# Optimization experiments

Measured on AMD Instinct MI355X. Metric: run time of the kernel, lower is better.

The kernel has to match this reference:

```python
import jax, jax.numpy as jnp
import numpy as np

K_FACTOR = 8
TOP_N = 4
NUM_LAYER = 2


def setup_inputs() -> dict:
    key = jax.random.key(0)
    ks = jax.random.split(key, 5)
    num_ent, num_rel, n_edges = 50000, 500, 500000
    emb_dim = 128
    emb_s = emb_dim // K_FACTOR  # 16
    ent_embeddings = jax.random.normal(ks[0], (num_ent, emb_dim), jnp.float32)
    rel_embeddings = jax.random.normal(ks[1], (num_rel, TOP_N * emb_s), jnp.float32)
    rel_att = jax.random.normal(ks[2], (num_rel, K_FACTOR), jnp.float32)
    edge_index = jax.random.randint(ks[3], (2, n_edges), 0, num_ent)
    edge_type = jax.random.randint(ks[4], (n_edges,), 0, num_rel)
    return dict(ent_embeddings=ent_embeddings, rel_embeddings=rel_embeddings,
                rel_att=rel_att, edge_index=edge_index, edge_type=edge_type,
                num_ent=num_ent, num_rel=num_rel)


def _segment_mean(src, idx, n):
    s = jax.ops.segment_sum(src, idx, num_segments=n)
    c = jax.ops.segment_sum(jnp.ones((src.shape[0],), src.dtype), idx, num_segments=n)
    return jnp.where(c[:, None] > 0, s / jnp.maximum(c, 1.0)[:, None], 0.0)


def _conv(x, r, r_att, ei, et, num_ent, num_rel):
    emb_dim = x.shape[1]
    s = emb_dim // K_FACTOR
    # add self-loop edges with relation id num_rel (zero embedding / zero att)
    loop = jnp.arange(num_ent, dtype=ei.dtype)
    ei = jnp.concatenate([ei, jnp.stack([loop, loop])], axis=1)
    et = jnp.concatenate([et, jnp.full((num_ent,), num_rel, et.dtype)])
    r_pad = jnp.concatenate([r, jnp.zeros((1, r.shape[1]), r.dtype)], axis=0)
    ra_pad = jnp.concatenate([r_att, jnp.zeros((1, K_FACTOR), r_att.dtype)], axis=0)

    neigh_t = x[ei[1]]          # (E, D)
    neigh_h = x[ei[0]]          # (E, D)
    neigh_r = r_pad[et]         # (E, top_n*s)
    att = jax.nn.softmax(ra_pad[et], axis=1)      # (E, k)
    order = jnp.argsort(-att, axis=-1)             # descending sort indices
    top, rem = order[:, :TOP_N], order[:, TOP_N:]

    E = neigh_h.shape[0]
    tf = neigh_t.reshape(E, K_FACTOR, s)
    hf = neigh_h.reshape(E, K_FACTOR, s)
    t_top = jnp.take_along_axis(tf, top[:, :, None], axis=1)  # (E, top_n, s)
    h_top = jnp.take_along_axis(hf, top[:, :, None], axis=1)
    h_rem = jnp.take_along_axis(hf, rem[:, :, None], axis=1)

    tmp = (h_top.reshape(E, -1) + neigh_r).reshape(E, TOP_N, s)
    rows = jnp.arange(E)[:, None]
    # the fresh random ent_embed in the original is fully overwritten by the
    # two scatters (top + remaining cover all k_factor slots) -> deterministic
    ent = (jnp.zeros((E, K_FACTOR, s), x.dtype)
           .at[rows, top].set(tmp)
           .at[rows, rem].set(h_rem))

    ent_embed = _segment_mean(ent.reshape(E, emb_dim), ei[1], num_ent)
    rel_embed = _segment_mean(t_top.reshape(E, -1) - h_top.reshape(E, -1), et, num_rel + 1)
    return jax.nn.relu(ent_embed), rel_embed[:-1], r_att


def reference(ent_embeddings, rel_embeddings, rel_att, edge_index, edge_type, num_ent, num_rel):
    x, r = ent_embeddings, rel_embeddings
    for _ in range(NUM_LAYER):
        # faithful to MAE.forward: the ORIGINAL rel_att is passed to every layer
        x, r, _ = _conv(x, r, rel_att, edge_index, edge_type, num_ent, num_rel)
    return (x, r)
```

## Files before the change

### kernel.cpp

```cpp
#include <hip/hip_runtime.h>

#define KF 8
#define TN 4
#define SDIM 16
#define EMB 128
#define NS 8
#define NB 128
#define NT 512
#define NRMAX 512
#define SCE 1024

typedef unsigned int u32;

__device__ __forceinline__ u32 pack2bf(float a, float b) {
    u32 ua = __float_as_uint(a), ub = __float_as_uint(b);
    ua = (ua + 0x7FFFu + ((ua >> 16) & 1u)) >> 16;
    ub = (ub + 0x7FFFu + ((ub >> 16) & 1u)) >> 16;
    return ua | (ub << 16);
}
__device__ __forceinline__ float lo16(u32 w) { return __uint_as_float(w << 16); }
__device__ __forceinline__ float hi16(u32 w) { return __uint_as_float(w & 0xFFFF0000u); }

__global__ __launch_bounds__(256) void k_init(int* __restrict__ deg, int num_ent,
                                              int* __restrict__ rcnt, int num_rel,
                                              float* __restrict__ rsumA, float* __restrict__ rsumB,
                                              int nrsum) {
    int i = blockIdx.x * 256 + threadIdx.x;
    if (i < num_ent) deg[i] = 0;
    if (i < num_rel) rcnt[i] = 0;
    if (i < nrsum) { rsumA[i] = 0.f; rsumB[i] = 0.f; }
}

__global__ __launch_bounds__(256) void k_hist(const int* __restrict__ tails, const int* __restrict__ types,
                                              int nE, int num_rel,
                                              int* __restrict__ deg, int* __restrict__ rcnt) {
    __shared__ int hist[NRMAX];
    for (int q = threadIdx.x; q < num_rel; q += 256) hist[q] = 0;
    __syncthreads();
    for (int i = blockIdx.x * 256 + threadIdx.x; i < nE; i += gridDim.x * 256) {
        atomicAdd(&deg[tails[i]], 1);
        atomicAdd(&hist[types[i]], 1);
    }
    __syncthreads();
    for (int q = threadIdx.x; q < num_rel; q += 256) {
        int h = hist[q];
        if (h) atomicAdd(&rcnt[q], h);
    }
}

__device__ void scan_small(const int* __restrict__ in, int* __restrict__ out, int* __restrict__ out2, int n) {
    __shared__ int warp_sums[16];
    int carry = 0;
    int lane = threadIdx.x & 63, wid = threadIdx.x >> 6;
    int nw = blockDim.x >> 6;
    for (int base = 0; base < n; base += blockDim.x) {
        int i = base + (int)threadIdx.x;
        int v = (i < n) ? in[i] : 0;
        int sv = v;
        for (int o = 1; o < 64; o <<= 1) { int t = __shfl_up(sv, o, 64); if (lane >= o) sv += t; }
        if (lane == 63) warp_sums[wid] = sv;
        __syncthreads();
        if (wid == 0 && lane < nw) {
            int ws = warp_sums[lane];
            for (int o = 1; o < 16; o <<= 1) { int t = __shfl_up(ws, o, 64); if (lane >= o) ws += t; }
            warp_sums[lane] = ws;
        }
        __syncthreads();
        int wofs = (wid > 0) ? warp_sums[wid - 1] : 0;
        int total = warp_sums[nw - 1];
        if (i < n) {
            int e = carry + wofs + sv - v;
            out[i] = e;
            if (out2) out2[i] = e;
        }
        carry += total;
        __syncthreads();
    }
    if (threadIdx.x == 0) out[n] = carry;
}

__global__ void k_scan_pair(const int* __restrict__ bsum, int* __restrict__ bofs, int nblk,
                            const int* __restrict__ rcnt, int* __restrict__ rel_off,
                            int* __restrict__ rel_cur, int num_rel) {
    if (blockIdx.x == 0) scan_small(bsum, bofs, nullptr, nblk);
    else                 scan_small(rcnt, rel_off, rel_cur, num_rel);
}

__global__ __launch_bounds__(256) void k_scan1(const int* __restrict__ in, int* __restrict__ out,
                                               int* __restrict__ bsum, int n) {
    __shared__ int warp_sums[4];
    int blk = blockIdx.x;
    int i0 = blk * SCE + (int)threadIdx.x * 4;
    int v[4];
#pragma unroll
    for (int j = 0; j < 4; ++j) { int i = i0 + j; v[j] = (i < n) ? in[i] : 0; }
    int tsum = v[0] + v[1] + v[2] + v[3];
    int lane = threadIdx.x & 63, wid = threadIdx.x >> 6;
    int sv = tsum;
    for (int o = 1; o < 64; o <<= 1) { int t = __shfl_up(sv, o, 64); if (lane >= o) sv += t; }
    if (lane == 63) warp_sums[wid] = sv;
    __syncthreads();
    if (threadIdx.x == 0) {
        int s = 0;
        for (int w = 0; w < 4; ++w) { int t = warp_sums[w]; warp_sums[w] = s; s += t; }
        bsum[blk] = s;
    }
    __syncthreads();
    int run = warp_sums[wid] + sv - tsum;
#pragma unroll
    for (int j = 0; j < 4; ++j) { int i = i0 + j; if (i < n) out[i] = run; run += v[j]; }
}

__global__ __launch_bounds__(256) void k_scan2(int* __restrict__ out, int* __restrict__ out2,
                                               const int* __restrict__ bofs, int n, int nblk) {
    int blk = blockIdx.x;
    int add = bofs[blk];
    int i0 = blk * SCE + (int)threadIdx.x * 4;
#pragma unroll
    for (int j = 0; j < 4; ++j) {
        int i = i0 + j;
        if (i < n) { int val = out[i] + add; out[i] = val; out2[i] = val; }
    }
    if (blk == 0 && threadIdx.x == 0) out[n] = bofs[nblk];
}

__global__ __launch_bounds__(256) void k_scatter_fused(
        const int* __restrict__ heads, const int* __restrict__ tails, const int* __restrict__ types,
        int nE, int num_ent, int num_rel,
        int* __restrict__ tail_cur, u32* __restrict__ tail_edges,
        int* __restrict__ rel_cur, u32* __restrict__ rel_edges,
        const float4* __restrict__ x4, u32* __restrict__ xh, int n4,
        const float* __restrict__ rel_att, const float* __restrict__ r0,
        int* __restrict__ posmap, int* __restrict__ topmap, u32* __restrict__ pr0,
        int nc, int np) {
    int bid = blockIdx.x;
    if (bid < NT) {
        int xcd = bid & 7;
        int w = bid >> 3;
        int nw = NT >> 3;
        int per = (num_ent + 7) >> 3;
        int lo = xcd * per, hi = min(lo + per, num_ent);
        for (int i = w * 256 + (int)threadIdx.x; i < nE; i += nw * 256) {
            int t = tails[i];
            if (t >= lo && t < hi) {
                int p = atomicAdd(&tail_cur[t], 1);
                tail_edges[p] = (u32)heads[i] | ((u32)types[i] << 16);
            }
        }
    } else if (bid < NT + NB) {
        __shared__ int hist[NRMAX];
        __shared__ int base[NRMAX];
        int bi = bid - NT;
        int c = (bi & 7) * (NB >> 3) + (bi >> 3);
        int chunk = (nE + NB - 1) / NB;
        int beg = c * chunk, end = min(beg + chunk, nE);
        for (int q = threadIdx.x; q < num_rel; q += 256) hist[q] = 0;
        __syncthreads();
        for (int i = beg + (int)threadIdx.x; i < end; i += 256) atomicAdd(&hist[types[i]], 1);
        __syncthreads();
        for (int q = threadIdx.x; q < num_rel; q += 256) {
            int h = hist[q];
            base[q] = h > 0 ? atomicAdd(&rel_cur[q], h) : 0;
            hist[q] = 0;
        }
        __syncthreads();
        for (int i = beg + (int)threadIdx.x; i < end; i += 256) {
            int q = types[i];
            int rank = atomicAdd(&hist[q], 1);
            rel_edges[base[q] + rank] = (u32)tails[i] | ((u32)heads[i] << 16);
        }
    } else if (bid < NT + NB + nc) {
        int i = (bid - NT - NB) * 256 + (int)threadIdx.x;
        if (i < n4) {
            float4 v = x4[i];
            ((uint2*)xh)[i] = make_uint2(pack2bf(v.x, v.y), pack2bf(v.z, v.w));
        }
    } else {
        int q = (bid - NT - NB - nc) * 4 + ((int)threadIdx.x >> 6);
        if (q >= num_rel) return;
        int i = threadIdx.x & 63;
        float v[KF]; int idx[KF];
        for (int k = 0; k < KF; ++k) { v[k] = rel_att[q * KF + k]; idx[k] = k; }
        for (int a = 1; a < KF; ++a) {
            float va = v[a]; int ia = idx[a]; int j = a - 1;
            while (j >= 0 && v[j] < va) { v[j + 1] = v[j]; idx[j + 1] = idx[j]; --j; }
            v[j + 1] = va; idx[j + 1] = ia;
        }
        int pos[KF];
        for (int k = 0; k < KF; ++k) pos[k] = -1;
        for (int j = 0; j < TN; ++j) pos[idx[j]] = j;
        if (i < KF) posmap[q * KF + i] = pos[i];
        if (i < TN) topmap[q * TN + i] = idx[i];
        int k = i >> 3;
        int p = pos[k];
        u32 w = 0;
        if (p >= 0) {
            float a = r0[q * 64 + p * SDIM + ((2 * i) & 15)];
            float b = r0[q * 64 + p * SDIM + ((2 * i + 1) & 15)];
            w = pack2bf(a, b);
        }
        pr0[q * 64 + i] = w;
    }
}

template <bool OUT_BF16>
__global__ __launch_bounds__(256) void k_layer(const u32* __restrict__ xh, const u32* __restrict__ prh,
                                               const int* __restrict__ tail_off,
                                               const u32* __restrict__ tail_edges,
                                               const int* __restrict__ rel_off,
                                               const u32* __restrict__ rel_edges,
                                               float* __restrict__ rsum,
                                               u32* __restrict__ xout_h, float4* __restrict__ xout_f,
                                               int num_ent, int num_rel) {
    int bid = blockIdx.x;
    int lane = threadIdx.x & 63;
    int qw = lane >> 4, c = lane & 15;
    int wid = threadIdx.x >> 6;
    if (bid < num_rel * NS) {
        int q = bid >> 3, s = bid & 7;
        int beg = rel_off[q], end = rel_off[q + 1];
        float acc[8] = {0.f, 0.f, 0.f, 0.f, 0.f, 0.f, 0.f, 0.f};
        int g = s * 4 + wid;
        for (int b2 = beg + g * 64; b2 < end; b2 += 32 * 64) {
            int m = min(64, end - b2);
            u32 ew = (lane < m) ? rel_edges[b2 + lane] : 0u;
            for (int j = 0; j < m; j += 4) {
                int idx = j + qw;
                u32 w = __shfl(ew, idx, 64);
                uint4 ta = make_uint4(0, 0, 0, 0), hb = make_uint4(0, 0, 0, 0);
                if (idx < m) {
                    int t = (int)(w & 0xFFFFu);
                    int h = (int)(w >> 16);
                    ta = *(const uint4*)(xh + ((size_t)t << 6) + (c << 2));
                    hb = *(const uint4*)(xh + ((size_t)h << 6) + (c << 2));
                }
                acc[0] += lo16(ta.x) - lo16(hb.x);
                acc[1] += hi16(ta.x) - hi16(hb.x);
                acc[2] += lo16(ta.y) - lo16(hb.y);
                acc[3] += hi16(ta.y) - hi16(hb.y);
                acc[4] += lo16(ta.z) - lo16(hb.z);
                acc[5] += hi16(ta.z) - hi16(hb.z);
                acc[6] += lo16(ta.w) - lo16(hb.w);
                acc[7] += hi16(ta.w) - hi16(hb.w);
            }
        }
#pragma unroll
        for (int d = 0; d < 8; ++d) {
            acc[d] += __shfl_xor(acc[d], 16, 64);
            acc[d] += __shfl_xor(acc[d], 32, 64);
        }
        __shared__ float prt[4][EMB];
        if (qw == 0) {
#pragma unroll
            for (int d = 0; d < 8; ++d) prt[wid][c * 8 + d] = acc[d];
        }
        __syncthreads();
        int tid = threadIdx.x;
        if (tid < EMB) {
            float v = prt[0][tid] + prt[1][tid] + prt[2][tid] + prt[3][tid];
            atomicAdd(&rsum[(size_t)q * EMB + tid], v);
        }
    } else {
        int t = (bid - num_rel * NS) * 4 + wid;
        if (t >= num_ent) return;
        int beg = tail_off[t], end = tail_off[t + 1];
        int deg = end - beg;
        float acc[8] = {0.f, 0.f, 0.f, 0.f, 0.f, 0.f, 0.f, 0.f};
        for (int b2 = 0; b2 < deg; b2 += 64) {
            int m = min(64, deg - b2);
            u32 ew = (lane < m) ? tail_edges[beg + b2 + lane] : 0u;
            for (int j = 0; j < m; j += 4) {
                int idx = j + qw;
                u32 w = __shfl(ew, idx, 64);
                uint4 xr = make_uint4(0, 0, 0, 0), pr = make_uint4(0, 0, 0, 0);
                if (idx < m) {
                    int h = (int)(w & 0xFFFFu);
                    int q = (int)(w >> 16);
                    xr = *(const uint4*)(xh + ((size_t)h << 6) + (c << 2));
                    pr = *(const uint4*)(prh + ((size_t)q << 6) + (c << 2));
                }
                acc[0] += lo16(xr.x) + lo16(pr.x);
                acc[1] += hi16(xr.x) + hi16(pr.x);
                acc[2] += lo16(xr.y) + lo16(pr.y);
                acc[3] += hi16(xr.y) + hi16(pr.y);
                acc[4] += lo16(xr.z) + lo16(pr.z);
                acc[5] += hi16(xr.z) + hi16(pr.z);
                acc[6] += lo16(xr.w) + lo16(pr.w);
                acc[7] += hi16(xr.w) + hi16(pr.w);
            }
        }
#pragma unroll
        for (int d = 0; d < 8; ++d) {
            acc[d] += __shfl_xor(acc[d], 16, 64);
            acc[d] += __shfl_xor(acc[d], 32, 64);
        }
        if (qw == 0) {
            uint4 sw = *(const uint4*)(xh + ((size_t)t << 6) + (c << 2));
            float s[8] = { lo16(sw.x), hi16(sw.x), lo16(sw.y), hi16(sw.y),
                           lo16(sw.z), hi16(sw.z), lo16(sw.w), hi16(sw.w) };
            float inv = 1.f / (float)(deg + 1);
            float o[8];
#pragma unroll
            for (int d = 0; d < 8; ++d) {
                float v = (acc[d] + s[d]) * inv;
                o[d] = v > 0.f ? v : 0.f;
            }
            if (OUT_BF16) {
                uint4 ow = make_uint4(pack2bf(o[0], o[1]), pack2bf(o[2], o[3]),
                                      pack2bf(o[4], o[5]), pack2bf(o[6], o[7]));
                *(uint4*)(xout_h + ((size_t)t << 6) + (c << 2)) = ow;
            } else {
                xout_f[((size_t)t << 5) + (c << 1)]     = make_float4(o[0], o[1], o[2], o[3]);
                xout_f[((size_t)t << 5) + (c << 1) + 1] = make_float4(o[4], o[5], o[6], o[7]);
            }
        }
    }
}

__global__ __launch_bounds__(64) void k_relfin_pr(const float* __restrict__ rsum,
                                                  const int* __restrict__ rel_off,
                                                  const int* __restrict__ posmap,
                                                  u32* __restrict__ prh, int num_rel) {
    int q = blockIdx.x;
    if (q >= num_rel) return;
    int i = threadIdx.x;
    int k = i >> 3;
    int pos = posmap[q * KF + k];
    int cnt = rel_off[q + 1] - rel_off[q];
    u32 w = 0;
    if (pos >= 0 && cnt > 0) {
        float inv = 1.f / (float)cnt;
        w = pack2bf(rsum[(size_t)q * EMB + 2 * i] * inv, rsum[(size_t)q * EMB + 2 * i + 1] * inv);
    }
    prh[q * 64 + i] = w;
}

__global__ __launch_bounds__(64) void k_relfin(const float* __restrict__ rsum,
                                               const int* __restrict__ rel_off,
                                               const int* __restrict__ topmap,
                                               float* __restrict__ rout) {
    int q = blockIdx.x;
    int t = threadIdx.x;
    int cnt = rel_off[q + 1] - rel_off[q];
    int j = t >> 4, sd = t & 15;
    int k = topmap[q * TN + j];
    float v = cnt > 0 ? rsum[(size_t)q * EMB + k * SDIM + sd] / (float)cnt : 0.f;
    rout[q * (TN * SDIM) + t] = v;
}

extern "C" void kernel_launch(void* const* d_in, const int* in_sizes, int n_in,
                              void* d_out, int out_size, void* d_ws, size_t ws_size,
                              hipStream_t stream) {
    const float* x0 = (const float*)d_in[0];
    const float* r0 = (const float*)d_in[1];
    const float* rel_att = (const float*)d_in[2];
    const int* edge_index = (const int*)d_in[3];
    const int* edge_type = (const int*)d_in[4];

    const int num_ent = in_sizes[0] / EMB;
    const int num_rel = in_sizes[2] / KF;
    const int nE = in_sizes[4];

    const int* heads = edge_index;
    const int* tails = edge_index + nE;

    const int nblk = (num_ent + SCE - 1) / SCE;
    const int n4 = num_ent * 32;
    const int nc = (n4 + 255) / 256;
    const int np = (num_rel + 3) / 4;

    char* base = (char*)d_ws;
    size_t off = 0;
    auto carve = [&](size_t bytes) { char* p = base + off; off = (off + bytes + 255) & ~(size_t)255; return p; };
    int* deg        = (int*)carve((size_t)num_ent * 4);
    int* tail_off   = (int*)carve((size_t)(num_ent + 1) * 4);
    int* tail_cur   = (int*)carve((size_t)num_ent * 4);
    u32* tail_edges = (u32*)carve((size_t)nE * 4);
    int* rcnt       = (int*)carve((size_t)num_rel * 4);
    int* rel_off    = (int*)carve((size_t)(num_rel + 1) * 4);
    int* rel_cur    = (int*)carve((size_t)num_rel * 4);
    u32* rel_edges  = (u32*)carve((size_t)nE * 4);
    int* posmap     = (int*)carve((size_t)num_rel * KF * 4);
    int* topmap     = (int*)carve((size_t)num_rel * TN * 4);
    int* bsum       = (int*)carve((size_t)nblk * 4);
    int* bofs       = (int*)carve((size_t)(nblk + 1) * 4);
    u32* x0h        = (u32*)carve((size_t)num_ent * EMB * 2);
    u32* x1h        = (u32*)carve((size_t)num_ent * EMB * 2);
    u32* pr0        = (u32*)carve((size_t)num_rel * 64 * 4);
    u32* pr1        = (u32*)carve((size_t)num_rel * 64 * 4);
    float* rsumA    = (float*)carve((size_t)num_rel * EMB * 4);
    float* rsumB    = (float*)carve((size_t)num_rel * EMB * 4);
    (void)ws_size;

    float* x_out = (float*)d_out;
    float* r_out = (float*)d_out + (size_t)num_ent * EMB;

    int initmax = num_ent > num_rel * EMB ? num_ent : num_rel * EMB;
    k_init<<<(initmax + 255) / 256, 256, 0, stream>>>(deg, num_ent, rcnt, num_rel,
                                                      rsumA, rsumB, num_rel * EMB);
    k_hist<<<256, 256, 0, stream>>>(tails, edge_type, nE, num_rel, deg, rcnt);
    k_scan1<<<nblk, 256, 0, stream>>>(deg, tail_off, bsum, num_ent);
    k_scan_pair<<<2, 1024, 0, stream>>>(bsum, bofs, nblk, rcnt, rel_off, rel_cur, num_rel);
    k_scan2<<<nblk, 256, 0, stream>>>(tail_off, tail_cur, bofs, num_ent, nblk);
    k_scatter_fused<<<NT + NB + nc + np, 256, 0, stream>>>(
        heads, tails, edge_type, nE, num_ent, num_rel,
        tail_cur, tail_edges, rel_cur, rel_edges,
        (const float4*)x0, x0h, n4, rel_att, r0, posmap, topmap, pr0, nc, np);

    int lgrid = num_rel * NS + (num_ent + 3) / 4;

    k_layer<true><<<lgrid, 256, 0, stream>>>(x0h, pr0, tail_off, tail_edges, rel_off, rel_edges,
                                             rsumA, x1h, nullptr, num_ent, num_rel);
    k_relfin_pr<<<num_rel, 64, 0, stream>>>(rsumA, rel_off, posmap, pr1, num_rel);

    k_layer<false><<<lgrid, 256, 0, stream>>>(x1h, pr1, tail_off, tail_edges, rel_off, rel_edges,
                                              rsumB, nullptr, (float4*)x_out, num_ent, num_rel);
    k_relfin<<<num_rel, 64, 0, stream>>>(rsumB, rel_off, topmap, r_out);
}
```

Baseline: 232.2 us.

## Split fused layer kernel into relation and entity passes, unroll gather loop by two

The combined per-layer kernel, which branched on block index between relation-sum blocks and entity-aggregation blocks, is split into two separate kernels launched back to back. Each edge loop now handles two edges per quarter-wave per iteration, so two independent gathers are in flight at once. The split gives each kernel its own register allocation and removes the divergent branch, but adds a launch per layer and serializes the two passes instead of letting their blocks run concurrently.

```diff
diff --git a/kernel.cpp b/kernel.cpp
--- a/kernel.cpp
+++ b/kernel.cpp
@@ -203,116 +203,127 @@
     }
 }
 
-template <bool OUT_BF16>
-__global__ __launch_bounds__(256) void k_layer(const u32* __restrict__ xh, const u32* __restrict__ prh,
-                                               const int* __restrict__ tail_off,
-                                               const u32* __restrict__ tail_edges,
-                                               const int* __restrict__ rel_off,
-                                               const u32* __restrict__ rel_edges,
-                                               float* __restrict__ rsum,
-                                               u32* __restrict__ xout_h, float4* __restrict__ xout_f,
-                                               int num_ent, int num_rel) {
+__global__ __launch_bounds__(256) void k_rel_pass(const u32* __restrict__ xh,
+                                                  const int* __restrict__ rel_off,
+                                                  const u32* __restrict__ rel_edges,
+                                                  float* __restrict__ rsum) {
     int bid = blockIdx.x;
+    int q = bid >> 3, s = bid & 7;
     int lane = threadIdx.x & 63;
     int qw = lane >> 4, c = lane & 15;
     int wid = threadIdx.x >> 6;
-    if (bid < num_rel * NS) {
-        int q = bid >> 3, s = bid & 7;
-        int beg = rel_off[q], end = rel_off[q + 1];
-        float acc[8] = {0.f, 0.f, 0.f, 0.f, 0.f, 0.f, 0.f, 0.f};
-        int g = s * 4 + wid;
-        for (int b2 = beg + g * 64; b2 < end; b2 += 32 * 64) {
-            int m = min(64, end - b2);
-            u32 ew = (lane < m) ? rel_edges[b2 + lane] : 0u;
-            for (int j = 0; j < m; j += 4) {
-                int idx = j + qw;
-                u32 w = __shfl(ew, idx, 64);
-                uint4 ta = make_uint4(0, 0, 0, 0), hb = make_uint4(0, 0, 0, 0);
-                if (idx < m) {
-                    int t = (int)(w & 0xFFFFu);
-                    int h = (int)(w >> 16);
-                    ta = *(const uint4*)(xh + ((size_t)t << 6) + (c << 2));
-                    hb = *(const uint4*)(xh + ((size_t)h << 6) + (c << 2));
-                }
-                acc[0] += lo16(ta.x) - lo16(hb.x);
-                acc[1] += hi16(ta.x) - hi16(hb.x);
-                acc[2] += lo16(ta.y) - lo16(hb.y);
-                acc[3] += hi16(ta.y) - hi16(hb.y);
-                acc[4] += lo16(ta.z) - lo16(hb.z);
-                acc[5] += hi16(ta.z) - hi16(hb.z);
-                acc[6] += lo16(ta.w) - lo16(hb.w);
-                acc[7] += hi16(ta.w) - hi16(hb.w);
+    int beg = rel_off[q], end = rel_off[q + 1];
+    float acc[8] = {0.f, 0.f, 0.f, 0.f, 0.f, 0.f, 0.f, 0.f};
+    int g = s * 4 + wid;
+    for (int b2 = beg + g * 64; b2 < end; b2 += 32 * 64) {
+        int m = min(64, end - b2);
+        u32 ew = (lane < m) ? rel_edges[b2 + lane] : 0u;
+        for (int j = 0; j < m; j += 8) {
+            int i0 = j + qw, i1 = j + qw + 4;
+            u32 w0 = __shfl(ew, i0, 64);
+            u32 w1 = __shfl(ew, i1, 64);
+            uint4 ta0 = make_uint4(0,0,0,0), hb0 = make_uint4(0,0,0,0);
+            uint4 ta1 = make_uint4(0,0,0,0), hb1 = make_uint4(0,0,0,0);
+            if (i0 < m) {
+                ta0 = *(const uint4*)(xh + ((size_t)(w0 & 0xFFFFu) << 6) + (c << 2));
+                hb0 = *(const uint4*)(xh + ((size_t)(w0 >> 16) << 6) + (c << 2));
             }
-        }
+            if (i1 < m) {
+                ta1 = *(const uint4*)(xh + ((size_t)(w1 & 0xFFFFu) << 6) + (c << 2));
+                hb1 = *(const uint4*)(xh + ((size_t)(w1 >> 16) << 6) + (c << 2));
+            }
+            acc[0] += (lo16(ta0.x) - lo16(hb0.x)) + (lo16(ta1.x) - lo16(hb1.x));
+            acc[1] += (hi16(ta0.x) - hi16(hb0.x)) + (hi16(ta1.x) - hi16(hb1.x));
+            acc[2] += (lo16(ta0.y) - lo16(hb0.y)) + (lo16(ta1.y) - lo16(hb1.y));
+            acc[3] += (hi16(ta0.y) - hi16(hb0.y)) + (hi16(ta1.y) - hi16(hb1.y));
+            acc[4] += (lo16(ta0.z) - lo16(hb0.z)) + (lo16(ta1.z) - lo16(hb1.z));
+            acc[5] += (hi16(ta0.z) - hi16(hb0.z)) + (hi16(ta1.z) - hi16(hb1.z));
+            acc[6] += (lo16(ta0.w) - lo16(hb0.w)) + (lo16(ta1.w) - lo16(hb1.w));
+            acc[7] += (hi16(ta0.w) - hi16(hb0.w)) + (hi16(ta1.w) - hi16(hb1.w));
+        }
+    }
+#pragma unroll
+    for (int d = 0; d < 8; ++d) {
+        acc[d] += __shfl_xor(acc[d], 16, 64);
+        acc[d] += __shfl_xor(acc[d], 32, 64);
+    }
+    __shared__ float prt[4][EMB];
+    if (qw == 0) {
+#pragma unroll
+        for (int d = 0; d < 8; ++d) prt[wid][c * 8 + d] = acc[d];
+    }
+    __syncthreads();
+    int tid = threadIdx.x;
+    if (tid < EMB) {
+        float v = prt[0][tid] + prt[1][tid] + prt[2][tid] + prt[3][tid];
+        atomicAdd(&rsum[(size_t)q * EMB + tid], v);
+    }
+}
+
+template <bool OUT_BF16>
+__global__ __launch_bounds__(256) void k_ent_pass(const u32* __restrict__ xh, const u32* __restrict__ prh,
+                                                  const int* __restrict__ tail_off,
+                                                  const u32* __restrict__ tail_edges,
+                                                  u32* __restrict__ xout_h, float4* __restrict__ xout_f,
+                                                  int num_ent) {
+    int wid = threadIdx.x >> 6;
+    int t = blockIdx.x * 4 + wid;
+    if (t >= num_ent) return;
+    int lane = threadIdx.x & 63;
+    int qw = lane >> 4, c = lane & 15;
+    int beg = tail_off[t], end = tail_off[t + 1];
+    int deg = end - beg;
+    float acc[8] = {0.f, 0.f, 0.f, 0.f, 0.f, 0.f, 0.f, 0.f};
+    for (int b2 = 0; b2 < deg; b2 += 64) {
+        int m = min(64, deg - b2);
+        u32 ew = (lane < m) ? tail_edges[beg + b2 + lane] : 0u;
+        for (int j = 0; j < m; j += 8) {
+            int i0 = j + qw, i1 = j + qw + 4;
+            u32 w0 = __shfl(ew, i0, 64);
+            u32 w1 = __shfl(ew, i1, 64);
+            uint4 xr0 = make_uint4(0,0,0,0), pr0 = make_uint4(0,0,0,0);
+            uint4 xr1 = make_uint4(0,0,0,0), pr1 = make_uint4(0,0,0,0);
+            if (i0 < m) {
+                xr0 = *(const uint4*)(xh + ((size_t)(w0 & 0xFFFFu) << 6) + (c << 2));
+                pr0 = *(const uint4*)(prh + ((size_t)(w0 >> 16) << 6) + (c << 2));
+            }
+            if (i1 < m) {
+                xr1 = *(const uint4*)(xh + ((size_t)(w1 & 0xFFFFu) << 6) + (c << 2));
+                pr1 = *(const uint4*)(prh + ((size_t)(w1 >> 16) << 6) + (c << 2));
+            }
+            acc[0] += (lo16(xr0.x) + lo16(pr0.x)) + (lo16(xr1.x) + lo16(pr1.x));
+            acc[1] += (hi16(xr0.x) + hi16(pr0.x)) + (hi16(xr1.x) + hi16(pr1.x));
+            acc[2] += (lo16(xr0.y) + lo16(pr0.y)) + (lo16(xr1.y) + lo16(pr1.y));
+            acc[3] += (hi16(xr0.y) + hi16(pr0.y)) + (hi16(xr1.y) + hi16(pr1.y));
+            acc[4] += (lo16(xr0.z) + lo16(pr0.z)) + (lo16(xr1.z) + lo16(pr1.z));
+            acc[5] += (hi16(xr0.z) + hi16(pr0.z)) + (hi16(xr1.z) + hi16(pr1.z));
+            acc[6] += (lo16(xr0.w) + lo16(pr0.w)) + (lo16(xr1.w) + lo16(pr1.w));
+            acc[7] += (hi16(xr0.w) + hi16(pr0.w)) + (hi16(xr1.w) + hi16(pr1.w));
+        }
+    }
+#pragma unroll
+    for (int d = 0; d < 8; ++d) {
+        acc[d] += __shfl_xor(acc[d], 16, 64);
+        acc[d] += __shfl_xor(acc[d], 32, 64);
+    }
+    if (qw == 0) {
+        uint4 sw = *(const uint4*)(xh + ((size_t)t << 6) + (c << 2));
+        float s[8] = { lo16(sw.x), hi16(sw.x), lo16(sw.y), hi16(sw.y),
+                       lo16(sw.z), hi16(sw.z), lo16(sw.w), hi16(sw.w) };
+        float inv = 1.f / (float)(deg + 1);
+        float o[8];
 #pragma unroll
         for (int d = 0; d < 8; ++d) {
-            acc[d] += __shfl_xor(acc[d], 16, 64);
-            acc[d] += __shfl_xor(acc[d], 32, 64);
-        }
-        __shared__ float prt[4][EMB];
-        if (qw == 0) {
-#pragma unroll
-            for (int d = 0; d < 8; ++d) prt[wid][c * 8 + d] = acc[d];
-        }
-        __syncthreads();
-        int tid = threadIdx.x;
-        if (tid < EMB) {
-            float v = prt[0][tid] + prt[1][tid] + prt[2][tid] + prt[3][tid];
-            atomicAdd(&rsum[(size_t)q * EMB + tid], v);
-        }
-    } else {
-        int t = (bid - num_rel * NS) * 4 + wid;
-        if (t >= num_ent) return;
-        int beg = tail_off[t], end = tail_off[t + 1];
-        int deg = end - beg;
-        float acc[8] = {0.f, 0.f, 0.f, 0.f, 0.f, 0.f, 0.f, 0.f};
-        for (int b2 = 0; b2 < deg; b2 += 64) {
-            int m = min(64, deg - b2);
-            u32 ew = (lane < m) ? tail_edges[beg + b2 + lane] : 0u;
-            for (int j = 0; j < m; j += 4) {
-                int idx = j + qw;
-                u32 w = __shfl(ew, idx, 64);
-                uint4 xr = make_uint4(0, 0, 0, 0), pr = make_uint4(0, 0, 0, 0);
-                if (idx < m) {
-                    int h = (int)(w & 0xFFFFu);
-                    int q = (int)(w >> 16);
-                    xr = *(const uint4*)(xh + ((size_t)h << 6) + (c << 2));
-                    pr = *(const uint4*)(prh + ((size_t)q << 6) + (c << 2));
-                }
-                acc[0] += lo16(xr.x) + lo16(pr.x);
-                acc[1] += hi16(xr.x) + hi16(pr.x);
-                acc[2] += lo16(xr.y) + lo16(pr.y);
-                acc[3] += hi16(xr.y) + hi16(pr.y);
-                acc[4] += lo16(xr.z) + lo16(pr.z);
-                acc[5] += hi16(xr.z) + hi16(pr.z);
-                acc[6] += lo16(xr.w) + lo16(pr.w);
-                acc[7] += hi16(xr.w) + hi16(pr.w);
-            }
-        }
-#pragma unroll
-        for (int d = 0; d < 8; ++d) {
-            acc[d] += __shfl_xor(acc[d], 16, 64);
-            acc[d] += __shfl_xor(acc[d], 32, 64);
-        }
-        if (qw == 0) {
-            uint4 sw = *(const uint4*)(xh + ((size_t)t << 6) + (c << 2));
-            float s[8] = { lo16(sw.x), hi16(sw.x), lo16(sw.y), hi16(sw.y),
-                           lo16(sw.z), hi16(sw.z), lo16(sw.w), hi16(sw.w) };
-            float inv = 1.f / (float)(deg + 1);
-            float o[8];
-#pragma unroll
-            for (int d = 0; d < 8; ++d) {
-                float v = (acc[d] + s[d]) * inv;
-                o[d] = v > 0.f ? v : 0.f;
-            }
-            if (OUT_BF16) {
-                uint4 ow = make_uint4(pack2bf(o[0], o[1]), pack2bf(o[2], o[3]),
-                                      pack2bf(o[4], o[5]), pack2bf(o[6], o[7]));
-                *(uint4*)(xout_h + ((size_t)t << 6) + (c << 2)) = ow;
-            } else {
-                xout_f[((size_t)t << 5) + (c << 1)]     = make_float4(o[0], o[1], o[2], o[3]);
-                xout_f[((size_t)t << 5) + (c << 1) + 1] = make_float4(o[4], o[5], o[6], o[7]);
-            }
+            float v = (acc[d] + s[d]) * inv;
+            o[d] = v > 0.f ? v : 0.f;
+        }
+        if (OUT_BF16) {
+            uint4 ow = make_uint4(pack2bf(o[0], o[1]), pack2bf(o[2], o[3]),
+                                  pack2bf(o[4], o[5]), pack2bf(o[6], o[7]));
+            *(uint4*)(xout_h + ((size_t)t << 6) + (c << 2)) = ow;
+        } else {
+            xout_f[((size_t)t << 5) + (c << 1)]     = make_float4(o[0], o[1], o[2], o[3]);
+            xout_f[((size_t)t << 5) + (c << 1) + 1] = make_float4(o[4], o[5], o[6], o[7]);
         }
     }
 }
@@ -407,13 +418,13 @@
         tail_cur, tail_edges, rel_cur, rel_edges,
         (const float4*)x0, x0h, n4, rel_att, r0, posmap, topmap, pr0, nc, np);
 
-    int lgrid = num_rel * NS + (num_ent + 3) / 4;
-
-    k_layer<true><<<lgrid, 256, 0, stream>>>(x0h, pr0, tail_off, tail_edges, rel_off, rel_edges,
-                                             rsumA, x1h, nullptr, num_ent, num_rel);
+    int egrid = (num_ent + 3) / 4;
+
+    k_rel_pass<<<num_rel * NS, 256, 0, stream>>>(x0h, rel_off, rel_edges, rsumA);
+    k_ent_pass<true><<<egrid, 256, 0, stream>>>(x0h, pr0, tail_off, tail_edges, x1h, nullptr, num_ent);
     k_relfin_pr<<<num_rel, 64, 0, stream>>>(rsumA, rel_off, posmap, pr1, num_rel);
 
-    k_layer<false><<<lgrid, 256, 0, stream>>>(x1h, pr1, tail_off, tail_edges, rel_off, rel_edges,
-                                              rsumB, nullptr, (float4*)x_out, num_ent, num_rel);
+    k_rel_pass<<<num_rel * NS, 256, 0, stream>>>(x1h, rel_off, rel_edges, rsumB);
+    k_ent_pass<false><<<egrid, 256, 0, stream>>>(x1h, pr1, tail_off, tail_edges, nullptr, (float4*)x_out, num_ent);
     k_relfin<<<num_rel, 64, 0, stream>>>(rsumB, rel_off, topmap, r_out);
 }
```

Result: no change. 234.1 us (+0.8%).

## Split layer kernel and gather only top-factor slices in relation pass

Applied to the files above, without the earlier changes.

The relation aggregation now gathers only the 4 top-ranked 16-wide factor slices (64 values) per edge, selected through topmap, instead of the full 128-dim rows. This halves the gather traffic and the accumulator size in that pass. The fused relation/entity layer kernel is also split into two separate kernels, a relation pass and an entity pass. The split adds one launch per layer and removes the overlap between the two branches that the single grid allowed.

```diff
diff --git a/kernel.cpp b/kernel.cpp
--- a/kernel.cpp
+++ b/kernel.cpp
@@ -203,121 +203,114 @@
     }
 }
 
-template <bool OUT_BF16>
-__global__ __launch_bounds__(256) void k_layer(const u32* __restrict__ xh, const u32* __restrict__ prh,
-                                               const int* __restrict__ tail_off,
-                                               const u32* __restrict__ tail_edges,
-                                               const int* __restrict__ rel_off,
-                                               const u32* __restrict__ rel_edges,
-                                               float* __restrict__ rsum,
-                                               u32* __restrict__ xout_h, float4* __restrict__ xout_f,
-                                               int num_ent, int num_rel) {
+__global__ __launch_bounds__(256) void k_rel_pass(const u32* __restrict__ xh,
+                                                  const int* __restrict__ rel_off,
+                                                  const u32* __restrict__ rel_edges,
+                                                  const int* __restrict__ topmap,
+                                                  float* __restrict__ rsum_top) {
     int bid = blockIdx.x;
+    int q = bid >> 3, s = bid & 7;
     int lane = threadIdx.x & 63;
     int qw = lane >> 4, c = lane & 15;
     int wid = threadIdx.x >> 6;
-    if (bid < num_rel * NS) {
-        int q = bid >> 3, s = bid & 7;
-        int beg = rel_off[q], end = rel_off[q + 1];
-        float acc[8] = {0.f, 0.f, 0.f, 0.f, 0.f, 0.f, 0.f, 0.f};
-        int g = s * 4 + wid;
-        for (int b2 = beg + g * 64; b2 < end; b2 += 32 * 64) {
-            int m = min(64, end - b2);
-            u32 ew = (lane < m) ? rel_edges[b2 + lane] : 0u;
-            for (int j = 0; j < m; j += 4) {
-                int idx = j + qw;
-                u32 w = __shfl(ew, idx, 64);
-                uint4 ta = make_uint4(0, 0, 0, 0), hb = make_uint4(0, 0, 0, 0);
-                if (idx < m) {
-                    int t = (int)(w & 0xFFFFu);
-                    int h = (int)(w >> 16);
-                    ta = *(const uint4*)(xh + ((size_t)t << 6) + (c << 2));
-                    hb = *(const uint4*)(xh + ((size_t)h << 6) + (c << 2));
-                }
-                acc[0] += lo16(ta.x) - lo16(hb.x);
-                acc[1] += hi16(ta.x) - hi16(hb.x);
-                acc[2] += lo16(ta.y) - lo16(hb.y);
-                acc[3] += hi16(ta.y) - hi16(hb.y);
-                acc[4] += lo16(ta.z) - lo16(hb.z);
-                acc[5] += hi16(ta.z) - hi16(hb.z);
-                acc[6] += lo16(ta.w) - lo16(hb.w);
-                acc[7] += hi16(ta.w) - hi16(hb.w);
+    int k = topmap[q * TN + (c >> 2)];
+    int woff = k * 8 + (c & 3) * 2;
+    int beg = rel_off[q], end = rel_off[q + 1];
+    float acc[4] = {0.f, 0.f, 0.f, 0.f};
+    for (int e = beg + s * 16 + wid * 4 + qw; e < end; e += 128) {
+        u32 ew = rel_edges[e];
+        int t = (int)(ew & 0xFFFFu);
+        int h = (int)(ew >> 16);
+        uint2 ta = *(const uint2*)(xh + ((size_t)t << 6) + woff);
+        uint2 hb = *(const uint2*)(xh + ((size_t)h << 6) + woff);
+        acc[0] += lo16(ta.x) - lo16(hb.x);
+        acc[1] += hi16(ta.x) - hi16(hb.x);
+        acc[2] += lo16(ta.y) - lo16(hb.y);
+        acc[3] += hi16(ta.y) - hi16(hb.y);
+    }
+#pragma unroll
+    for (int d = 0; d < 4; ++d) {
+        acc[d] += __shfl_xor(acc[d], 16, 64);
+        acc[d] += __shfl_xor(acc[d], 32, 64);
+    }
+    __shared__ float prt[4][64];
+    if (qw == 0) {
+#pragma unroll
+        for (int d = 0; d < 4; ++d) prt[wid][c * 4 + d] = acc[d];
+    }
+    __syncthreads();
+    int tid = threadIdx.x;
+    if (tid < 64) {
+        float v = prt[0][tid] + prt[1][tid] + prt[2][tid] + prt[3][tid];
+        atomicAdd(&rsum_top[(size_t)q * 64 + tid], v);
+    }
+}
+
+template <bool OUT_BF16>
+__global__ __launch_bounds__(256) void k_ent_pass(const u32* __restrict__ xh, const u32* __restrict__ prh,
+                                                  const int* __restrict__ tail_off,
+                                                  const u32* __restrict__ tail_edges,
+                                                  u32* __restrict__ xout_h, float4* __restrict__ xout_f,
+                                                  int num_ent) {
+    int wid = threadIdx.x >> 6;
+    int t = blockIdx.x * 4 + wid;
+    if (t >= num_ent) return;
+    int lane = threadIdx.x & 63;
+    int qw = lane >> 4, c = lane & 15;
+    int beg = tail_off[t], end = tail_off[t + 1];
+    int deg = end - beg;
+    float acc[8] = {0.f, 0.f, 0.f, 0.f, 0.f, 0.f, 0.f, 0.f};
+    for (int b2 = 0; b2 < deg; b2 += 64) {
+        int m = min(64, deg - b2);
+        u32 ew = (lane < m) ? tail_edges[beg + b2 + lane] : 0u;
+        for (int j = 0; j < m; j += 4) {
+            int idx = j + qw;
+            u32 w = __shfl(ew, idx, 64);
+            uint4 xr = make_uint4(0, 0, 0, 0), pr = make_uint4(0, 0, 0, 0);
+            if (idx < m) {
+                int h = (int)(w & 0xFFFFu);
+                int q = (int)(w >> 16);
+                xr = *(const uint4*)(xh + ((size_t)h << 6) + (c << 2));
+                pr = *(const uint4*)(prh + ((size_t)q << 6) + (c << 2));
             }
-        }
+            acc[0] += lo16(xr.x) + lo16(pr.x);
+            acc[1] += hi16(xr.x) + hi16(pr.x);
+            acc[2] += lo16(xr.y) + lo16(pr.y);
+            acc[3] += hi16(xr.y) + hi16(pr.y);
+            acc[4] += lo16(xr.z) + lo16(pr.z);
+            acc[5] += hi16(xr.z) + hi16(pr.z);
+            acc[6] += lo16(xr.w) + lo16(pr.w);
+            acc[7] += hi16(xr.w) + hi16(pr.w);
+        }
+    }
+#pragma unroll
+    for (int d = 0; d < 8; ++d) {
+        acc[d] += __shfl_xor(acc[d], 16, 64);
+        acc[d] += __shfl_xor(acc[d], 32, 64);
+    }
+    if (qw == 0) {
+        uint4 sw = *(const uint4*)(xh + ((size_t)t << 6) + (c << 2));
+        float s[8] = { lo16(sw.x), hi16(sw.x), lo16(sw.y), hi16(sw.y),
+                       lo16(sw.z), hi16(sw.z), lo16(sw.w), hi16(sw.w) };
+        float inv = 1.f / (float)(deg + 1);
+        float o[8];
 #pragma unroll
         for (int d = 0; d < 8; ++d) {
-            acc[d] += __shfl_xor(acc[d], 16, 64);
-            acc[d] += __shfl_xor(acc[d], 32, 64);
-        }
-        __shared__ float prt[4][EMB];
-        if (qw == 0) {
-#pragma unroll
-            for (int d = 0; d < 8; ++d) prt[wid][c * 8 + d] = acc[d];
-        }
-        __syncthreads();
-        int tid = threadIdx.x;
-        if (tid < EMB) {
-            float v = prt[0][tid] + prt[1][tid] + prt[2][tid] + prt[3][tid];
-            atomicAdd(&rsum[(size_t)q * EMB + tid], v);
-        }
-    } else {
-        int t = (bid - num_rel * NS) * 4 + wid;
-        if (t >= num_ent) return;
-        int beg = tail_off[t], end = tail_off[t + 1];
-        int deg = end - beg;
-        float acc[8] = {0.f, 0.f, 0.f, 0.f, 0.f, 0.f, 0.f, 0.f};
-        for (int b2 = 0; b2 < deg; b2 += 64) {
-            int m = min(64, deg - b2);
-            u32 ew = (lane < m) ? tail_edges[beg + b2 + lane] : 0u;
-            for (int j = 0; j < m; j += 4) {
-                int idx = j + qw;
-                u32 w = __shfl(ew, idx, 64);
-                uint4 xr = make_uint4(0, 0, 0, 0), pr = make_uint4(0, 0, 0, 0);
-                if (idx < m) {
-                    int h = (int)(w & 0xFFFFu);
-                    int q = (int)(w >> 16);
-                    xr = *(const uint4*)(xh + ((size_t)h << 6) + (c << 2));
-                    pr = *(const uint4*)(prh + ((size_t)q << 6) + (c << 2));
-                }
-                acc[0] += lo16(xr.x) + lo16(pr.x);
-                acc[1] += hi16(xr.x) + hi16(pr.x);
-                acc[2] += lo16(xr.y) + lo16(pr.y);
-                acc[3] += hi16(xr.y) + hi16(pr.y);
-                acc[4] += lo16(xr.z) + lo16(pr.z);
-                acc[5] += hi16(xr.z) + hi16(pr.z);
-                acc[6] += lo16(xr.w) + lo16(pr.w);
-                acc[7] += hi16(xr.w) + hi16(pr.w);
-            }
-        }
-#pragma unroll
-        for (int d = 0; d < 8; ++d) {
-            acc[d] += __shfl_xor(acc[d], 16, 64);
-            acc[d] += __shfl_xor(acc[d], 32, 64);
-        }
-        if (qw == 0) {
-            uint4 sw = *(const uint4*)(xh + ((size_t)t << 6) + (c << 2));
-            float s[8] = { lo16(sw.x), hi16(sw.x), lo16(sw.y), hi16(sw.y),
-                           lo16(sw.z), hi16(sw.z), lo16(sw.w), hi16(sw.w) };
-            float inv = 1.f / (float)(deg + 1);
-            float o[8];
-#pragma unroll
-            for (int d = 0; d < 8; ++d) {
-                float v = (acc[d] + s[d]) * inv;
-                o[d] = v > 0.f ? v : 0.f;
-            }
-            if (OUT_BF16) {
-                uint4 ow = make_uint4(pack2bf(o[0], o[1]), pack2bf(o[2], o[3]),
-                                      pack2bf(o[4], o[5]), pack2bf(o[6], o[7]));
-                *(uint4*)(xout_h + ((size_t)t << 6) + (c << 2)) = ow;
-            } else {
-                xout_f[((size_t)t << 5) + (c << 1)]     = make_float4(o[0], o[1], o[2], o[3]);
-                xout_f[((size_t)t << 5) + (c << 1) + 1] = make_float4(o[4], o[5], o[6], o[7]);
-            }
-        }
-    }
-}
-
-__global__ __launch_bounds__(64) void k_relfin_pr(const float* __restrict__ rsum,
+            float v = (acc[d] + s[d]) * inv;
+            o[d] = v > 0.f ? v : 0.f;
+        }
+        if (OUT_BF16) {
+            uint4 ow = make_uint4(pack2bf(o[0], o[1]), pack2bf(o[2], o[3]),
+                                  pack2bf(o[4], o[5]), pack2bf(o[6], o[7]));
+            *(uint4*)(xout_h + ((size_t)t << 6) + (c << 2)) = ow;
+        } else {
+            xout_f[((size_t)t << 5) + (c << 1)]     = make_float4(o[0], o[1], o[2], o[3]);
+            xout_f[((size_t)t << 5) + (c << 1) + 1] = make_float4(o[4], o[5], o[6], o[7]);
+        }
+    }
+}
+
+__global__ __launch_bounds__(64) void k_relfin_pr(const float* __restrict__ rsum_top,
                                                   const int* __restrict__ rel_off,
                                                   const int* __restrict__ posmap,
                                                   u32* __restrict__ prh, int num_rel) {
@@ -330,22 +323,21 @@
     u32 w = 0;
     if (pos >= 0 && cnt > 0) {
         float inv = 1.f / (float)cnt;
-        w = pack2bf(rsum[(size_t)q * EMB + 2 * i] * inv, rsum[(size_t)q * EMB + 2 * i + 1] * inv);
+        int d0 = (2 * i) & 15;
+        float a = rsum_top[(size_t)q * 64 + pos * SDIM + d0] * inv;
+        float b = rsum_top[(size_t)q * 64 + pos * SDIM + d0 + 1] * inv;
+        w = pack2bf(a, b);
     }
     prh[q * 64 + i] = w;
 }
 
-__global__ __launch_bounds__(64) void k_relfin(const float* __restrict__ rsum,
+__global__ __launch_bounds__(64) void k_relfin(const float* __restrict__ rsum_top,
                                                const int* __restrict__ rel_off,
-                                               const int* __restrict__ topmap,
                                                float* __restrict__ rout) {
     int q = blockIdx.x;
     int t = threadIdx.x;
     int cnt = rel_off[q + 1] - rel_off[q];
-    int j = t >> 4, sd = t & 15;
-    int k = topmap[q * TN + j];
-    float v = cnt > 0 ? rsum[(size_t)q * EMB + k * SDIM + sd] / (float)cnt : 0.f;
-    rout[q * (TN * SDIM) + t] = v;
+    rout[q * 64 + t] = cnt > 0 ? rsum_top[(size_t)q * 64 + t] / (float)cnt : 0.f;
 }
 
 extern "C" void kernel_launch(void* const* d_in, const int* in_sizes, int n_in,
@@ -388,16 +380,16 @@
     u32* x1h        = (u32*)carve((size_t)num_ent * EMB * 2);
     u32* pr0        = (u32*)carve((size_t)num_rel * 64 * 4);
     u32* pr1        = (u32*)carve((size_t)num_rel * 64 * 4);
-    float* rsumA    = (float*)carve((size_t)num_rel * EMB * 4);
-    float* rsumB    = (float*)carve((size_t)num_rel * EMB * 4);
+    float* rsumA    = (float*)carve((size_t)num_rel * 64 * 4);
+    float* rsumB    = (float*)carve((size_t)num_rel * 64 * 4);
     (void)ws_size;
 
     float* x_out = (float*)d_out;
     float* r_out = (float*)d_out + (size_t)num_ent * EMB;
 
-    int initmax = num_ent > num_rel * EMB ? num_ent : num_rel * EMB;
+    int initmax = num_ent > num_rel * 64 ? num_ent : num_rel * 64;
     k_init<<<(initmax + 255) / 256, 256, 0, stream>>>(deg, num_ent, rcnt, num_rel,
-                                                      rsumA, rsumB, num_rel * EMB);
+                                                      rsumA, rsumB, num_rel * 64);
     k_hist<<<256, 256, 0, stream>>>(tails, edge_type, nE, num_rel, deg, rcnt);
     k_scan1<<<nblk, 256, 0, stream>>>(deg, tail_off, bsum, num_ent);
     k_scan_pair<<<2, 1024, 0, stream>>>(bsum, bofs, nblk, rcnt, rel_off, rel_cur, num_rel);
@@ -407,13 +399,13 @@
         tail_cur, tail_edges, rel_cur, rel_edges,
         (const float4*)x0, x0h, n4, rel_att, r0, posmap, topmap, pr0, nc, np);
 
-    int lgrid = num_rel * NS + (num_ent + 3) / 4;
-
-    k_layer<true><<<lgrid, 256, 0, stream>>>(x0h, pr0, tail_off, tail_edges, rel_off, rel_edges,
-                                             rsumA, x1h, nullptr, num_ent, num_rel);
+    int egrid = (num_ent + 3) / 4;
+
+    k_rel_pass<<<num_rel * NS, 256, 0, stream>>>(x0h, rel_off, rel_edges, topmap, rsumA);
+    k_ent_pass<true><<<egrid, 256, 0, stream>>>(x0h, pr0, tail_off, tail_edges, x1h, nullptr, num_ent);
     k_relfin_pr<<<num_rel, 64, 0, stream>>>(rsumA, rel_off, posmap, pr1, num_rel);
 
-    k_layer<false><<<lgrid, 256, 0, stream>>>(x1h, pr1, tail_off, tail_edges, rel_off, rel_edges,
-                                              rsumB, nullptr, (float4*)x_out, num_ent, num_rel);
-    k_relfin<<<num_rel, 64, 0, stream>>>(rsumB, rel_off, topmap, r_out);
-}
+    k_rel_pass<<<num_rel * NS, 256, 0, stream>>>(x1h, rel_off, rel_edges, topmap, rsumB);
+    k_ent_pass<false><<<egrid, 256, 0, stream>>>(x1h, pr1, tail_off, tail_edges, nullptr, (float4*)x_out, num_ent);
+    k_relfin<<<num_rel, 64, 0, stream>>>(rsumB, rel_off, r_out);
+}
```

Measured after the change: 195.7 us. 1.19x faster.
